# Kernel optimization log

Measured on AMD Instinct MI355X. Metric: run time of the kernel, lower is better.

Reference implementation:

```python
import jax, jax.numpy as jnp
import numpy as np

L, B, D = 4096, 4, 512  # seq_len, batch, embed_dim (nhead=1 so kdim=vdim=D)


def setup_inputs() -> dict:
    key = jax.random.key(0)
    ks = jax.random.split(key, 11)
    sc = 1.0 / np.sqrt(D)
    return {
        "x": jax.random.normal(ks[0], (L, B, D), jnp.float32),
        "e": jax.random.normal(ks[1], (L, B, D), jnp.float32),
        "relay": jax.random.normal(ks[2], (1, B, D), jnp.float32),
        "Wq": jax.random.normal(ks[3], (D, D), jnp.float32) * sc,
        "bq": jax.random.normal(ks[4], (D,), jnp.float32) * sc,
        "Wk": jax.random.normal(ks[5], (D, D), jnp.float32) * sc,
        "bk": jax.random.normal(ks[6], (D,), jnp.float32) * sc,
        "Wv": jax.random.normal(ks[7], (D, D), jnp.float32) * sc,
        "bv": jax.random.normal(ks[8], (D,), jnp.float32) * sc,
        "Wo": jax.random.normal(ks[9], (D, D), jnp.float32) * sc,
        "bo": jax.random.normal(ks[10], (D,), jnp.float32) * sc,
    }


def _window3(t):
    # t: [L,B,D] -> [L,B,3,D] with zero padding at the sequence boundaries
    # (matches nn.Unfold(kernel=[3,1], padding=[1,0]): positions l-1, l, l+1)
    n = t.shape[0]
    tp = jnp.pad(t, ((1, 1), (0, 0), (0, 0)))
    return jnp.stack([tp[:n], tp[1:n + 1], tp[2:n + 2]], axis=2)


def reference(x, e, relay, Wq, bq, Wk, bk, Wv, bv, Wo, bo):
    l, b, d = x.shape
    scale = 1.0 / jnp.sqrt(jnp.asarray(d, x.dtype))

    q = x @ Wq.T + bq          # [L,B,D]
    k = x @ Wk.T + bk
    v = x @ Wv.T + bv

    # cores = [embedding tokens e ; relay broadcast over L]  -> [2,L,B,D]
    s = jnp.broadcast_to(relay, (l, b, d))
    cores = jnp.stack([e, s], axis=0)
    k_c = cores @ Wk.T + bk    # [2,L,B,D]
    v_c = cores @ Wv.T + bv

    # ring (local windowed) attention: window = [k_{l-1},k_l,k_{l+1}, k(e_l), k(relay)]
    kw = jnp.concatenate([_window3(k), jnp.transpose(k_c, (1, 2, 0, 3))], axis=2)  # [L,B,5,D]
    vw = jnp.concatenate([_window3(v), jnp.transpose(v_c, (1, 2, 0, 3))], axis=2)  # [L,B,5,D]
    logits = jnp.einsum('lbd,lbwd->lbw', q, kw) * scale
    alphas = jax.nn.softmax(logits, axis=2)
    ring = jnp.einsum('lbw,lbwd->lbd', alphas, vw)  # [L,B,D]

    # star (relay) attention: query is the UNprojected relay token (as in source)
    k_r = relay @ Wk.T + bk    # [1,B,D]
    v_r = relay @ Wv.T + bv
    kk = jnp.concatenate([k, k_r], axis=0)  # [L+1,B,D]
    vv = jnp.concatenate([v, v_r], axis=0)
    s_logits = jnp.einsum('obd,nbd->bon', relay, kk) * scale  # [B,1,L+1]
    s_alphas = jax.nn.softmax(s_logits, axis=-1)
    star = jnp.einsum('bon,nbd->obd', s_alphas, vv)  # [1,B,D]

    return (ring @ Wo.T + bo, star @ Wo.T + bo)
```

## Files before the change

kernel.cpp:

```cpp
#include <hip/hip_runtime.h>
#include <hip/hip_fp16.h>

#define L_SEQ 4096
#define BATCH 4
#define DIM 512
#define M_ROWS (L_SEQ * BATCH)
#define SCALE 0.04419417382415922f
#define SLS 4097

typedef __attribute__((ext_vector_type(4))) float f32x4;
typedef __attribute__((ext_vector_type(8))) _Float16 f16x8;
typedef __attribute__((ext_vector_type(4))) _Float16 f16x4;

__device__ inline void gload16(const void* g, void* l) {
    __builtin_amdgcn_global_load_lds(
        (const __attribute__((address_space(1))) void*)g,
        (__attribute__((address_space(3))) void*)l, 16, 0, 0);
}

__device__ inline float wred_sum(float s) {
#pragma unroll
    for (int o = 32; o; o >>= 1) s += __shfl_xor(s, o);
    return s;
}
__device__ inline float wred_max(float s) {
#pragma unroll
    for (int o = 32; o; o >>= 1) s = fmaxf(s, __shfl_xor(s, o));
    return s;
}

#define PREP_NV   1048576
#define PREP_XE_B 8192
#define PREP_W_B  768
__global__ __launch_bounds__(256) void prep(
    const float* __restrict__ x, const float* __restrict__ e,
    const float* __restrict__ Wq, const float* __restrict__ Wk,
    const float* __restrict__ Wv, const float* __restrict__ Wo,
    const float* __restrict__ bq, const float* __restrict__ bk, const float* __restrict__ bv,
    const float* __restrict__ relay,
    _Float16* __restrict__ xh, _Float16* __restrict__ eh,
    _Float16* __restrict__ Wqkv, _Float16* __restrict__ Wof, float* __restrict__ bqkv,
    float* __restrict__ krvr, float* __restrict__ star)
{
    const int bid = blockIdx.x;
    if (bid < PREP_XE_B) {
        int j = bid * 256 + threadIdx.x;
        const float* src; _Float16* dst;
        if (j < PREP_NV) { src = x; dst = xh; } else { src = e; dst = eh; j -= PREP_NV; }
        const float* p = src + (size_t)j * 8;
        float4 a = *(const float4*)p, b = *(const float4*)(p + 4);
        f16x8 h = { (_Float16)a.x, (_Float16)a.y, (_Float16)a.z, (_Float16)a.w,
                    (_Float16)b.x, (_Float16)b.y, (_Float16)b.z, (_Float16)b.w };
        *(f16x8*)(dst + (size_t)j * 8) = h;
    } else if (bid < PREP_XE_B + PREP_W_B) {
        const int w = (bid - PREP_XE_B) * 256 + threadIdx.x;
        const int o = w * 4, r = o >> 9, c = o & 511;
        const float* W = (r < 512) ? Wq : (r < 1024 ? Wk : Wv);
        float4 v = *(const float4*)(W + (size_t)(r & 511) * 512 + c);
        *(f16x4*)(Wqkv + o) = f16x4{ (_Float16)v.x, (_Float16)v.y, (_Float16)v.z, (_Float16)v.w };
        if (o < 262144) {
            float4 u = *(const float4*)(Wo + o);
            *(f16x4*)(Wof + o) = f16x4{ (_Float16)u.x, (_Float16)u.y, (_Float16)u.z, (_Float16)u.w };
        }
        if (w < 1536) bqkv[w] = (w < 512) ? bq[w] : (w < 1024 ? bk[w - 512] : bv[w - 1024]);
    } else {
        const int o = ((bid - PREP_XE_B - PREP_W_B) << 2) + (threadIdx.x >> 6);
        const int lane = threadIdx.x & 63;
        const int sel = o >> 11, rem = o & 2047, b = rem >> 9, j = rem & 511;
        const float* W = sel ? Wv : Wk;
        const float* wr = W + (size_t)j * 512 + lane * 8;
        const float* rp = relay + (size_t)b * 512 + lane * 8;
        float4 w0 = *(const float4*)wr,  w1 = *(const float4*)(wr + 4);
        float4 r0 = *(const float4*)rp,  r1 = *(const float4*)(rp + 4);
        float s = w0.x * r0.x + w0.y * r0.y + w0.z * r0.z + w0.w * r0.w
                + w1.x * r1.x + w1.y * r1.y + w1.z * r1.z + w1.w * r1.w;
        s = wred_sum(s);
        if (lane == 0) {
            krvr[o] = s + (sel ? bv[j] : bk[j]);
            if (o < 2048) star[o] = 0.f;
        }
    }
}

struct GemmP {
    const _Float16* A;
    const _Float16* W;
    const float*    bias;
    void*           C;
    int             cstride;
    int             ncols;
};

template<int OUT16>
__global__ __launch_bounds__(256) void gemm2p(GemmP g0, GemmP g1, int n0, int cpx)
{
    __shared__ __align__(16) char smem[49152];
    _Float16* lAb = (_Float16*)smem;
    _Float16* lBb = (_Float16*)(smem + 24576);

    const int bid = blockIdx.x;
    const int swz = (bid & 7) * cpx + (bid >> 3);
    const GemmP g = (swz < n0) ? g0 : g1;
    const int l  = (swz < n0) ? swz : swz - n0;
    const int mt = l / g.ncols, nt = l % g.ncols;
    const int row0 = mt * 128, col0 = nt * 128;

    const int tid = threadIdx.x;
    const int wave = tid >> 6, lane = tid & 63;
    const int wm = (wave >> 1) * 64, wn = (wave & 1) * 64;

    f32x4 acc[4][4];
#pragma unroll
    for (int i = 0; i < 4; ++i)
#pragma unroll
        for (int j = 0; j < 4; ++j) acc[i][j] = (f32x4)0.f;

    const int idx0 = tid, idx1 = 256 + tid;
    const int r0_ = idx0 >> 2, c0_ = ((idx0 & 3) ^ ((idx0 >> 3) & 3)) * 8;
    const int r1_ = idx1 >> 2, c1_ = ((idx1 & 3) ^ ((idx1 >> 3) & 3)) * 8;
    const int ldsb0 = (wave * 64) * 8;
    const int ldsb1 = (256 + wave * 64) * 8;

    auto stage = [&](int buf, int t) {
        const int k0 = t << 5;
        gload16(g.A + (size_t)(row0 + r0_) * 512 + k0 + c0_, lAb + buf * 4096 + ldsb0);
        gload16(g.A + (size_t)(row0 + r1_) * 512 + k0 + c1_, lAb + buf * 4096 + ldsb1);
        gload16(g.W + (size_t)(col0 + r0_) * 512 + k0 + c0_, lBb + buf * 4096 + ldsb0);
        gload16(g.W + (size_t)(col0 + r1_) * 512 + k0 + c1_, lBb + buf * 4096 + ldsb1);
    };
    stage(0, 0);
    stage(1, 1);
    stage(2, 2);

    const int rslot = ((lane >> 4) ^ ((lane >> 1) & 3)) * 8;
    const int arb = (wm + (lane & 15)) * 32 + rslot;
    const int brb = (wn + (lane & 15)) * 32 + rslot;

    int rs = 0;
#pragma unroll 1
    for (int t = 0; t < 16; ++t) {
        if (t < 14)       asm volatile("s_waitcnt vmcnt(8)" ::: "memory");
        else if (t == 14) asm volatile("s_waitcnt vmcnt(4)" ::: "memory");
        else              asm volatile("s_waitcnt vmcnt(0)" ::: "memory");
        __builtin_amdgcn_s_barrier();
        f16x8 af[4], bfr[4];
#pragma unroll
        for (int i = 0; i < 4; ++i) af[i]  = *(const f16x8*)(lAb + rs * 4096 + arb + i * 512);
#pragma unroll
        for (int i = 0; i < 4; ++i) bfr[i] = *(const f16x8*)(lBb + rs * 4096 + brb + i * 512);
        __builtin_amdgcn_s_setprio(1);
#pragma unroll
        for (int mi = 0; mi < 4; ++mi)
#pragma unroll
            for (int ni = 0; ni < 4; ++ni)
                acc[mi][ni] = __builtin_amdgcn_mfma_f32_16x16x32_f16(
                    af[mi], bfr[ni], acc[mi][ni], 0, 0, 0);
        __builtin_amdgcn_s_setprio(0);
        asm volatile("s_waitcnt lgkmcnt(0)" ::: "memory");
        __builtin_amdgcn_s_barrier();
        if (t + 3 < 16) stage(rs, t + 3);
        rs = (rs == 2) ? 0 : rs + 1;
    }

    const int h = lane >> 4, c = lane & 15;
    if (OUT16) {
        _Float16* ep = (_Float16*)smem;
#pragma unroll
        for (int mi = 0; mi < 4; ++mi)
#pragma unroll
            for (int ni = 0; ni < 4; ++ni) {
                const float bb = g.bias[col0 + wn + ni * 16 + c];
#pragma unroll
                for (int r = 0; r < 4; ++r)
                    ep[(wm + mi * 16 + h * 4 + r) * 136 + wn + ni * 16 + c] =
                        (_Float16)(acc[mi][ni][r] + bb);
            }
        __syncthreads();
        const int rt = tid >> 4, ct = (tid & 15) * 8;
#pragma unroll
        for (int j = 0; j < 8; ++j) {
            const int row = j * 16 + rt;
            f16x8 v = *(const f16x8*)(ep + row * 136 + ct);
            *(f16x8*)((_Float16*)g.C + (size_t)(row0 + row) * g.cstride + col0 + ct) = v;
        }
    } else {
        float* ep = (float*)smem;
#pragma unroll
        for (int pass = 0; pass < 2; ++pass) {
            if ((wm == 0) == (pass == 0)) {
#pragma unroll
                for (int mi = 0; mi < 4; ++mi)
#pragma unroll
                    for (int ni = 0; ni < 4; ++ni) {
                        const float bb = g.bias[col0 + wn + ni * 16 + c];
#pragma unroll
                        for (int r = 0; r < 4; ++r)
                            ep[(mi * 16 + h * 4 + r) * 132 + wn + ni * 16 + c] =
                                acc[mi][ni][r] + bb;
                    }
            }
            __syncthreads();
            const int rt = tid >> 5, ct4 = (tid & 31) * 4;
#pragma unroll
            for (int j = 0; j < 8; ++j) {
                const int row = j * 8 + rt;
                f32x4 v = *(const f32x4*)(ep + row * 132 + ct4);
                *(f32x4*)((float*)g.C + (size_t)(row0 + pass * 64 + row) * g.cstride + col0 + ct4) = v;
            }
            if (pass == 0) __syncthreads();
        }
    }
}

__global__ __launch_bounds__(256) void tail_fused(GemmP g,
    const float* __restrict__ star, const float* __restrict__ Wo,
    const float* __restrict__ bo, float* __restrict__ out1)
{
    __shared__ __align__(16) char smem[49152];
    const int bid = blockIdx.x;
    const int tid = threadIdx.x;
    const int lane = tid & 63;

    if (bid >= 512) {
        const int o = ((bid - 512) << 2) + (tid >> 6);
        const int b = o >> 9, j = o & 511;
        const float* sp = star + (size_t)b * 512 + lane * 8;
        const float* wr = Wo + (size_t)j * 512 + lane * 8;
        float4 w0 = *(const float4*)wr,  w1 = *(const float4*)(wr + 4);
        float4 s0 = *(const float4*)sp,  s1 = *(const float4*)(sp + 4);
        float s = w0.x * s0.x + w0.y * s0.y + w0.z * s0.z + w0.w * s0.w
                + w1.x * s1.x + w1.y * s1.y + w1.z * s1.z + w1.w * s1.w;
        s = wred_sum(s);
        if (lane == 0) out1[o] = s + bo[j];
        return;
    }

    _Float16* lAb = (_Float16*)smem;
    _Float16* lBb = (_Float16*)(smem + 24576);

    const int swz = (bid & 7) * 64 + (bid >> 3);
    const int mt = swz / g.ncols, nt = swz % g.ncols;
    const int row0 = mt * 128, col0 = nt * 128;

    const int wave = tid >> 6;
    const int wm = (wave >> 1) * 64, wn = (wave & 1) * 64;

    f32x4 acc[4][4];
#pragma unroll
    for (int i = 0; i < 4; ++i)
#pragma unroll
        for (int j = 0; j < 4; ++j) acc[i][j] = (f32x4)0.f;

    const int idx0 = tid, idx1 = 256 + tid;
    const int r0_ = idx0 >> 2, c0_ = ((idx0 & 3) ^ ((idx0 >> 3) & 3)) * 8;
    const int r1_ = idx1 >> 2, c1_ = ((idx1 & 3) ^ ((idx1 >> 3) & 3)) * 8;
    const int ldsb0 = (wave * 64) * 8;
    const int ldsb1 = (256 + wave * 64) * 8;

    auto stage = [&](int buf, int t) {
        const int k0 = t << 5;
        gload16(g.A + (size_t)(row0 + r0_) * 512 + k0 + c0_, lAb + buf * 4096 + ldsb0);
        gload16(g.A + (size_t)(row0 + r1_) * 512 + k0 + c1_, lAb + buf * 4096 + ldsb1);
        gload16(g.W + (size_t)(col0 + r0_) * 512 + k0 + c0_, lBb + buf * 4096 + ldsb0);
        gload16(g.W + (size_t)(col0 + r1_) * 512 + k0 + c1_, lBb + buf * 4096 + ldsb1);
    };
    stage(0, 0);
    stage(1, 1);
    stage(2, 2);

    const int rslot = ((lane >> 4) ^ ((lane >> 1) & 3)) * 8;
    const int arb = (wm + (lane & 15)) * 32 + rslot;
    const int brb = (wn + (lane & 15)) * 32 + rslot;

    int rs = 0;
#pragma unroll 1
    for (int t = 0; t < 16; ++t) {
        if (t < 14)       asm volatile("s_waitcnt vmcnt(8)" ::: "memory");
        else if (t == 14) asm volatile("s_waitcnt vmcnt(4)" ::: "memory");
        else              asm volatile("s_waitcnt vmcnt(0)" ::: "memory");
        __builtin_amdgcn_s_barrier();
        f16x8 af[4], bfr[4];
#pragma unroll
        for (int i = 0; i < 4; ++i) af[i]  = *(const f16x8*)(lAb + rs * 4096 + arb + i * 512);
#pragma unroll
        for (int i = 0; i < 4; ++i) bfr[i] = *(const f16x8*)(lBb + rs * 4096 + brb + i * 512);
        __builtin_amdgcn_s_setprio(1);
#pragma unroll
        for (int mi = 0; mi < 4; ++mi)
#pragma unroll
            for (int ni = 0; ni < 4; ++ni)
                acc[mi][ni] = __builtin_amdgcn_mfma_f32_16x16x32_f16(
                    af[mi], bfr[ni], acc[mi][ni], 0, 0, 0);
        __builtin_amdgcn_s_setprio(0);
        asm volatile("s_waitcnt lgkmcnt(0)" ::: "memory");
        __builtin_amdgcn_s_barrier();
        if (t + 3 < 16) stage(rs, t + 3);
        rs = (rs == 2) ? 0 : rs + 1;
    }

    const int h = lane >> 4, c = lane & 15;
    float* ep = (float*)smem;
#pragma unroll
    for (int pass = 0; pass < 2; ++pass) {
        if ((wm == 0) == (pass == 0)) {
#pragma unroll
            for (int mi = 0; mi < 4; ++mi)
#pragma unroll
                for (int ni = 0; ni < 4; ++ni) {
                    const float bb = g.bias[col0 + wn + ni * 16 + c];
#pragma unroll
                    for (int r = 0; r < 4; ++r)
                        ep[(mi * 16 + h * 4 + r) * 132 + wn + ni * 16 + c] =
                            acc[mi][ni][r] + bb;
                }
        }
        __syncthreads();
        const int rt = tid >> 5, ct4 = (tid & 31) * 4;
#pragma unroll
        for (int j = 0; j < 8; ++j) {
            const int row = j * 8 + rt;
            f32x4 v = *(const f32x4*)(ep + row * 132 + ct4);
            *(f32x4*)((float*)g.C + (size_t)(row0 + pass * 64 + row) * g.cstride + col0 + ct4) = v;
        }
        if (pass == 0) __syncthreads();
    }
}

__global__ __launch_bounds__(256) void ring_attn(
    const _Float16* __restrict__ qkv,
    const _Float16* __restrict__ ekv,
    const float* __restrict__ krvr,
    const float* __restrict__ relay,
    _Float16* __restrict__ ring,
    float* __restrict__ slog)
{
    const int wid = (blockIdx.x << 2) + (threadIdx.x >> 6);
    const int lane = threadIdx.x & 63;
    const int r = wid, b = r & 3, l = r >> 2;
    const int d0 = lane << 3;

    float q[8], rl[8];
    {
        f16x8 t = *(const f16x8*)(qkv + (size_t)r * 1536 + d0);
#pragma unroll
        for (int i = 0; i < 8; ++i) q[i] = (float)t[i];
        const float* rp = relay + (size_t)b * 512 + d0;
        float4 a = *(const float4*)rp, c = *(const float4*)(rp + 4);
        rl[0] = a.x; rl[1] = a.y; rl[2] = a.z; rl[3] = a.w;
        rl[4] = c.x; rl[5] = c.y; rl[6] = c.z; rl[7] = c.w;
    }
    const bool has0 = (l > 0), has2 = (l < L_SEQ - 1);

    auto dotk = [&](const _Float16* kp) -> float {
        f16x8 t = *(const f16x8*)(kp + d0);
        float s = 0.f;
#pragma unroll
        for (int i = 0; i < 8; ++i) s += q[i] * (float)t[i];
        return wred_sum(s);
    };

    float lg[5];
    lg[0] = has0 ? dotk(qkv + (size_t)(r - 4) * 1536 + 512) : 0.f;
    lg[2] = has2 ? dotk(qkv + (size_t)(r + 4) * 1536 + 512) : 0.f;
    lg[3] = dotk(ekv + (size_t)r * 1024);
    {
        f16x8 t = *(const f16x8*)(qkv + (size_t)r * 1536 + 512 + d0);
        float s1 = 0.f, s2 = 0.f;
#pragma unroll
        for (int i = 0; i < 8; ++i) { float kf = (float)t[i]; s1 += q[i] * kf; s2 += rl[i] * kf; }
#pragma unroll
        for (int o = 32; o; o >>= 1) { s1 += __shfl_xor(s1, o); s2 += __shfl_xor(s2, o); }
        lg[1] = s1;
        if (lane == 0) slog[(size_t)b * SLS + l] = s2 * SCALE;
    }
    {
        const float* kp = krvr + (size_t)b * 512 + d0;
        float s = 0.f;
#pragma unroll
        for (int i = 0; i < 8; ++i) s += q[i] * kp[i];
        lg[4] = wred_sum(s);
    }

    float li[5], m = -1e30f;
#pragma unroll
    for (int w = 0; w < 5; ++w) { li[w] = lg[w] * SCALE; m = fmaxf(m, li[w]); }
    float ew[5], Z = 0.f;
#pragma unroll
    for (int w = 0; w < 5; ++w) { ew[w] = expf(li[w] - m); Z += ew[w]; }
    const float inv = 1.f / Z;

    float o8[8] = {0, 0, 0, 0, 0, 0, 0, 0};
    auto addv = [&](const _Float16* vp, float a) {
        f16x8 t = *(const f16x8*)(vp + d0);
#pragma unroll
        for (int i = 0; i < 8; ++i) o8[i] += a * (float)t[i];
    };
    if (has0) addv(qkv + (size_t)(r - 4) * 1536 + 1024, ew[0] * inv);
    addv(qkv + (size_t)r * 1536 + 1024, ew[1] * inv);
    if (has2) addv(qkv + (size_t)(r + 4) * 1536 + 1024, ew[2] * inv);
    addv(ekv + (size_t)r * 1024 + 512, ew[3] * inv);
    {
        const float* vp = krvr + 2048 + (size_t)b * 512 + d0;
        const float a = ew[4] * inv;
#pragma unroll
        for (int i = 0; i < 8; ++i) o8[i] += a * vp[i];
    }
    f16x8 res;
#pragma unroll
    for (int i = 0; i < 8; ++i) res[i] = (_Float16)o8[i];
    *(f16x8*)(ring + (size_t)r * 512 + d0) = res;
}

__global__ __launch_bounds__(1024) void star_softmax(
    const float* __restrict__ relay, const float* __restrict__ krvr,
    float* __restrict__ slog)
{
    const int b = blockIdx.x, t = threadIdx.x, lane = t & 63, w = t >> 6;
    __shared__ float red[16];
    __shared__ float bc[2];
    float* sl = slog + (size_t)b * SLS;

    float p = 0.f;
    if (t < 512) p = relay[(size_t)b * 512 + t] * krvr[(size_t)b * 512 + t];
    p = wred_sum(p);
    if (lane == 0) red[w] = p;
    __syncthreads();
    if (t == 0) { float s = 0.f; for (int i = 0; i < 16; ++i) s += red[i]; bc[0] = s * SCALE; }
    __syncthreads();
    const float selfl = bc[0];
    __syncthreads();

    float v[4];
#pragma unroll
    for (int i = 0; i < 4; ++i) v[i] = sl[t + i * 1024];

    float m = selfl;
#pragma unroll
    for (int i = 0; i < 4; ++i) m = fmaxf(m, v[i]);
    m = wred_max(m);
    if (lane == 0) red[w] = m;
    __syncthreads();
    if (t == 0) { float mm = red[0]; for (int i = 1; i < 16; ++i) mm = fmaxf(mm, red[i]); bc[1] = mm; }
    __syncthreads();
    m = bc[1];

    float ev[4], z = (t == 0) ? expf(selfl - m) : 0.f;
#pragma unroll
    for (int i = 0; i < 4; ++i) { ev[i] = expf(v[i] - m); z += ev[i]; }
    z = wred_sum(z);
    if (lane == 0) red[w] = z;
    __syncthreads();
    if (t == 0) { float s = 0.f; for (int i = 0; i < 16; ++i) s += red[i]; bc[0] = 1.f / s; }
    __syncthreads();
    const float inv = bc[0];

#pragma unroll
    for (int i = 0; i < 4; ++i) sl[t + i * 1024] = ev[i] * inv;
    if (t == 0) sl[SLS - 1] = expf(selfl - m) * inv;
}

__global__ __launch_bounds__(256) void star_out(
    const float* __restrict__ slog, const _Float16* __restrict__ qkv,
    const float* __restrict__ krvr, float* __restrict__ star)
{
    const int b = threadIdx.x >> 6, lane = threadIdx.x & 63;
    const int chunk = blockIdx.x;
    const int d0 = lane << 3;
    const float* al = slog + (size_t)b * SLS;
    float acc[8] = {0, 0, 0, 0, 0, 0, 0, 0};
#pragma unroll 4
    for (int i = 0; i < 64; ++i) {
        const int n = chunk * 64 + i;
        const float a = al[n];
        f16x8 v = *(const f16x8*)(qkv + (size_t)(n * 4 + b) * 1536 + 1024 + d0);
#pragma unroll
        for (int j = 0; j < 8; ++j) acc[j] += a * (float)v[j];
    }
    if (chunk == 63) {
        const float a = al[SLS - 1];
        const float* vr = krvr + 2048 + (size_t)b * 512 + d0;
#pragma unroll
        for (int j = 0; j < 8; ++j) acc[j] += a * vr[j];
    }
#pragma unroll
    for (int j = 0; j < 8; ++j) atomicAdd(&star[(size_t)b * 512 + d0 + j], acc[j]);
}

extern "C" void kernel_launch(void* const* d_in, const int* in_sizes, int n_in,
                              void* d_out, int out_size, void* d_ws, size_t ws_size,
                              hipStream_t stream) {
    const float* x     = (const float*)d_in[0];
    const float* e     = (const float*)d_in[1];
    const float* relay = (const float*)d_in[2];
    const float* Wq    = (const float*)d_in[3];
    const float* bq    = (const float*)d_in[4];
    const float* Wk    = (const float*)d_in[5];
    const float* bk    = (const float*)d_in[6];
    const float* Wv    = (const float*)d_in[7];
    const float* bv    = (const float*)d_in[8];
    const float* Wo    = (const float*)d_in[9];
    const float* bo    = (const float*)d_in[10];
    float* out = (float*)d_out;

    size_t off = 0;
    auto alloc = [&](size_t bytes) {
        void* p = (char*)d_ws + off;
        off += (bytes + 255) & ~(size_t)255;
        return p;
    };
    _Float16* Wqkv = (_Float16*)alloc((size_t)1536 * 512 * 2);
    _Float16* Wof  = (_Float16*)alloc((size_t)512 * 512 * 2);
    float*    bqkv = (float*)   alloc(1536 * 4);
    _Float16* xh   = (_Float16*)alloc((size_t)M_ROWS * 512 * 2);
    _Float16* eh   = (_Float16*)alloc((size_t)M_ROWS * 512 * 2);
    _Float16* qkv  = (_Float16*)alloc((size_t)M_ROWS * 1536 * 2);
    _Float16* ekv  = (_Float16*)alloc((size_t)M_ROWS * 1024 * 2);
    float*    krvr = (float*)   alloc(2 * 4 * 512 * 4);
    float*    slog = (float*)   alloc((size_t)4 * SLS * 4);
    float*    star = (float*)   alloc(4 * 512 * 4);
    _Float16* ringb = xh;

    prep<<<PREP_XE_B + PREP_W_B + 1024, 256, 0, stream>>>(
        x, e, Wq, Wk, Wv, Wo, bq, bk, bv, relay,
        xh, eh, Wqkv, Wof, bqkv, krvr, star);

    GemmP gq { xh, Wqkv,                     bqkv,       qkv, 1536, 12 };
    GemmP ge { eh, Wqkv + (size_t)512 * 512, bqkv + 512, ekv, 1024,  8 };
    gemm2p<1><<<2560, 256, 0, stream>>>(gq, ge, 1536, 320);

    ring_attn<<<M_ROWS / 4, 256, 0, stream>>>(qkv, ekv, krvr, relay, ringb, slog);

    star_softmax<<<4, 1024, 0, stream>>>(relay, krvr, slog);
    star_out<<<64, 256, 0, stream>>>(slog, qkv, krvr, star);

    GemmP go { ringb, Wof, bo, out, 512, 4 };
    tail_fused<<<1024, 256, 0, stream>>>(go, star, Wo, bo, out + (size_t)M_ROWS * 512);
}
```

Measured before the change: 151.1 us.

## Fuse fp32-to-fp16 activation conversion into QKV GEMM A-tile loading

Removes the separate prep pass that converted x and e to fp16. The QKV GEMM now loads fp32 A tiles into registers, converts them, and writes them to LDS inside a restructured three-slot software pipeline, while B tiles still use direct global-to-LDS loads. This avoids a full write and re-read of the fp16 activations. The cost is twice the global bytes for A in every GEMM tile, since each A row is re-read once per column tile, plus extra register pressure from the staged A buffers.

```diff
diff --git a/kernel.cpp b/kernel.cpp
--- a/kernel.cpp
+++ b/kernel.cpp
@@ -29,31 +29,17 @@
     return s;
 }
 
-#define PREP_NV   1048576
-#define PREP_XE_B 8192
-#define PREP_W_B  768
 __global__ __launch_bounds__(256) void prep(
-    const float* __restrict__ x, const float* __restrict__ e,
     const float* __restrict__ Wq, const float* __restrict__ Wk,
     const float* __restrict__ Wv, const float* __restrict__ Wo,
     const float* __restrict__ bq, const float* __restrict__ bk, const float* __restrict__ bv,
     const float* __restrict__ relay,
-    _Float16* __restrict__ xh, _Float16* __restrict__ eh,
     _Float16* __restrict__ Wqkv, _Float16* __restrict__ Wof, float* __restrict__ bqkv,
     float* __restrict__ krvr, float* __restrict__ star)
 {
     const int bid = blockIdx.x;
-    if (bid < PREP_XE_B) {
-        int j = bid * 256 + threadIdx.x;
-        const float* src; _Float16* dst;
-        if (j < PREP_NV) { src = x; dst = xh; } else { src = e; dst = eh; j -= PREP_NV; }
-        const float* p = src + (size_t)j * 8;
-        float4 a = *(const float4*)p, b = *(const float4*)(p + 4);
-        f16x8 h = { (_Float16)a.x, (_Float16)a.y, (_Float16)a.z, (_Float16)a.w,
-                    (_Float16)b.x, (_Float16)b.y, (_Float16)b.z, (_Float16)b.w };
-        *(f16x8*)(dst + (size_t)j * 8) = h;
-    } else if (bid < PREP_XE_B + PREP_W_B) {
-        const int w = (bid - PREP_XE_B) * 256 + threadIdx.x;
+    if (bid < 768) {
+        const int w = bid * 256 + threadIdx.x;
         const int o = w * 4, r = o >> 9, c = o & 511;
         const float* W = (r < 512) ? Wq : (r < 1024 ? Wk : Wv);
         float4 v = *(const float4*)(W + (size_t)(r & 511) * 512 + c);
@@ -64,7 +50,7 @@
         }
         if (w < 1536) bqkv[w] = (w < 512) ? bq[w] : (w < 1024 ? bk[w - 512] : bv[w - 1024]);
     } else {
-        const int o = ((bid - PREP_XE_B - PREP_W_B) << 2) + (threadIdx.x >> 6);
+        const int o = ((bid - 768) << 2) + (threadIdx.x >> 6);
         const int lane = threadIdx.x & 63;
         const int sel = o >> 11, rem = o & 2047, b = rem >> 9, j = rem & 511;
         const float* W = sel ? Wv : Wk;
@@ -83,7 +69,7 @@
 }
 
 struct GemmP {
-    const _Float16* A;
+    const void*     A;
     const _Float16* W;
     const float*    bias;
     void*           C;
@@ -108,6 +94,7 @@
     const int tid = threadIdx.x;
     const int wave = tid >> 6, lane = tid & 63;
     const int wm = (wave >> 1) * 64, wn = (wave & 1) * 64;
+    const float* Af = (const float*)g.A;
 
     f32x4 acc[4][4];
 #pragma unroll
@@ -115,39 +102,57 @@
 #pragma unroll
         for (int j = 0; j < 4; ++j) acc[i][j] = (f32x4)0.f;
 
-    const int idx0 = tid, idx1 = 256 + tid;
-    const int r0_ = idx0 >> 2, c0_ = ((idx0 & 3) ^ ((idx0 >> 3) & 3)) * 8;
+    const int idx1 = 256 + tid;
+    const int r0_ = tid >> 2,  c0_ = ((tid & 3) ^ ((tid >> 3) & 3)) * 8;
     const int r1_ = idx1 >> 2, c1_ = ((idx1 & 3) ^ ((idx1 >> 3) & 3)) * 8;
     const int ldsb0 = (wave * 64) * 8;
     const int ldsb1 = (256 + wave * 64) * 8;
 
-    auto stage = [&](int buf, int t) {
+    auto stageB = [&](int slot, int t) {
         const int k0 = t << 5;
-        gload16(g.A + (size_t)(row0 + r0_) * 512 + k0 + c0_, lAb + buf * 4096 + ldsb0);
-        gload16(g.A + (size_t)(row0 + r1_) * 512 + k0 + c1_, lAb + buf * 4096 + ldsb1);
-        gload16(g.W + (size_t)(col0 + r0_) * 512 + k0 + c0_, lBb + buf * 4096 + ldsb0);
-        gload16(g.W + (size_t)(col0 + r1_) * 512 + k0 + c1_, lBb + buf * 4096 + ldsb1);
-    };
-    stage(0, 0);
-    stage(1, 1);
-    stage(2, 2);
+        gload16(g.W + (size_t)(col0 + r0_) * 512 + k0 + c0_, lBb + slot * 4096 + ldsb0);
+        gload16(g.W + (size_t)(col0 + r1_) * 512 + k0 + c1_, lBb + slot * 4096 + ldsb1);
+    };
+    f32x4 a0[4], a1[4], a2[4];
+    auto loadA = [&](f32x4* d, int t) {
+        const int k0 = t << 5;
+        const float* p0 = Af + (size_t)(row0 + r0_) * 512 + k0 + c0_;
+        const float* p1 = Af + (size_t)(row0 + r1_) * 512 + k0 + c1_;
+        d[0] = *(const f32x4*)p0; d[1] = *(const f32x4*)(p0 + 4);
+        d[2] = *(const f32x4*)p1; d[3] = *(const f32x4*)(p1 + 4);
+    };
+    auto writeA = [&](const f32x4* s, int slot) {
+        f16x8 h0 = { (_Float16)s[0][0], (_Float16)s[0][1], (_Float16)s[0][2], (_Float16)s[0][3],
+                     (_Float16)s[1][0], (_Float16)s[1][1], (_Float16)s[1][2], (_Float16)s[1][3] };
+        f16x8 h1 = { (_Float16)s[2][0], (_Float16)s[2][1], (_Float16)s[2][2], (_Float16)s[2][3],
+                     (_Float16)s[3][0], (_Float16)s[3][1], (_Float16)s[3][2], (_Float16)s[3][3] };
+        *(f16x8*)(lAb + slot * 4096 + tid * 8) = h0;
+        *(f16x8*)(lAb + slot * 4096 + (256 + tid) * 8) = h1;
+    };
+
+    stageB(0, 0); stageB(1, 1); stageB(2, 2);
+    asm volatile("" ::: "memory");
+    loadA(a0, 0); asm volatile("" ::: "memory");
+    loadA(a1, 1); asm volatile("" ::: "memory");
+    loadA(a2, 2);
+    asm volatile("s_waitcnt vmcnt(8)" ::: "memory");
+    writeA(a0, 0);
+    asm volatile("s_waitcnt lgkmcnt(0)" ::: "memory");
 
     const int rslot = ((lane >> 4) ^ ((lane >> 1) & 3)) * 8;
     const int arb = (wm + (lane & 15)) * 32 + rslot;
     const int brb = (wn + (lane & 15)) * 32 + rslot;
 
-    int rs = 0;
-#pragma unroll 1
-    for (int t = 0; t < 16; ++t) {
-        if (t < 14)       asm volatile("s_waitcnt vmcnt(8)" ::: "memory");
-        else if (t == 14) asm volatile("s_waitcnt vmcnt(4)" ::: "memory");
-        else              asm volatile("s_waitcnt vmcnt(0)" ::: "memory");
+    auto step = [&](int t, int slot, int swrt, f32x4* aW, f32x4* aL) {
+        if (t == 0)      asm volatile("s_waitcnt vmcnt(4)" ::: "memory");
+        else if (t < 14) asm volatile("s_waitcnt vmcnt(6)" ::: "memory");
+        else             asm volatile("s_waitcnt vmcnt(0)" ::: "memory");
         __builtin_amdgcn_s_barrier();
         f16x8 af[4], bfr[4];
 #pragma unroll
-        for (int i = 0; i < 4; ++i) af[i]  = *(const f16x8*)(lAb + rs * 4096 + arb + i * 512);
-#pragma unroll
-        for (int i = 0; i < 4; ++i) bfr[i] = *(const f16x8*)(lBb + rs * 4096 + brb + i * 512);
+        for (int i = 0; i < 4; ++i) af[i]  = *(const f16x8*)(lAb + slot * 4096 + arb + i * 512);
+#pragma unroll
+        for (int i = 0; i < 4; ++i) bfr[i] = *(const f16x8*)(lBb + slot * 4096 + brb + i * 512);
         __builtin_amdgcn_s_setprio(1);
 #pragma unroll
         for (int mi = 0; mi < 4; ++mi)
@@ -156,11 +161,22 @@
                 acc[mi][ni] = __builtin_amdgcn_mfma_f32_16x16x32_f16(
                     af[mi], bfr[ni], acc[mi][ni], 0, 0, 0);
         __builtin_amdgcn_s_setprio(0);
+        if (t < 15) writeA(aW, swrt);
         asm volatile("s_waitcnt lgkmcnt(0)" ::: "memory");
         __builtin_amdgcn_s_barrier();
-        if (t + 3 < 16) stage(rs, t + 3);
-        rs = (rs == 2) ? 0 : rs + 1;
-    }
+        if (t <= 12) {
+            stageB(slot, t + 3);
+            asm volatile("" ::: "memory");
+            loadA(aL, t + 3);
+        }
+    };
+#pragma unroll 1
+    for (int tb = 0; tb < 15; tb += 3) {
+        step(tb,     0, 1, a1, a0);
+        step(tb + 1, 1, 2, a2, a1);
+        step(tb + 2, 2, 0, a0, a2);
+    }
+    step(15, 0, 1, a1, a0);
 
     const int h = lane >> 4, c = lane & 15;
     if (OUT16) {
@@ -237,6 +253,7 @@
 
     _Float16* lAb = (_Float16*)smem;
     _Float16* lBb = (_Float16*)(smem + 24576);
+    const _Float16* Ah = (const _Float16*)g.A;
 
     const int swz = (bid & 7) * 64 + (bid >> 3);
     const int mt = swz / g.ncols, nt = swz % g.ncols;
@@ -259,8 +276,8 @@
 
     auto stage = [&](int buf, int t) {
         const int k0 = t << 5;
-        gload16(g.A + (size_t)(row0 + r0_) * 512 + k0 + c0_, lAb + buf * 4096 + ldsb0);
-        gload16(g.A + (size_t)(row0 + r1_) * 512 + k0 + c1_, lAb + buf * 4096 + ldsb1);
+        gload16(Ah + (size_t)(row0 + r0_) * 512 + k0 + c0_, lAb + buf * 4096 + ldsb0);
+        gload16(Ah + (size_t)(row0 + r1_) * 512 + k0 + c1_, lAb + buf * 4096 + ldsb1);
         gload16(g.W + (size_t)(col0 + r0_) * 512 + k0 + c0_, lBb + buf * 4096 + ldsb0);
         gload16(g.W + (size_t)(col0 + r1_) * 512 + k0 + c1_, lBb + buf * 4096 + ldsb1);
     };
@@ -511,21 +528,19 @@
     _Float16* Wqkv = (_Float16*)alloc((size_t)1536 * 512 * 2);
     _Float16* Wof  = (_Float16*)alloc((size_t)512 * 512 * 2);
     float*    bqkv = (float*)   alloc(1536 * 4);
-    _Float16* xh   = (_Float16*)alloc((size_t)M_ROWS * 512 * 2);
-    _Float16* eh   = (_Float16*)alloc((size_t)M_ROWS * 512 * 2);
     _Float16* qkv  = (_Float16*)alloc((size_t)M_ROWS * 1536 * 2);
     _Float16* ekv  = (_Float16*)alloc((size_t)M_ROWS * 1024 * 2);
+    _Float16* ringb= (_Float16*)alloc((size_t)M_ROWS * 512 * 2);
     float*    krvr = (float*)   alloc(2 * 4 * 512 * 4);
     float*    slog = (float*)   alloc((size_t)4 * SLS * 4);
     float*    star = (float*)   alloc(4 * 512 * 4);
-    _Float16* ringb = xh;
-
-    prep<<<PREP_XE_B + PREP_W_B + 1024, 256, 0, stream>>>(
-        x, e, Wq, Wk, Wv, Wo, bq, bk, bv, relay,
-        xh, eh, Wqkv, Wof, bqkv, krvr, star);
-
-    GemmP gq { xh, Wqkv,                     bqkv,       qkv, 1536, 12 };
-    GemmP ge { eh, Wqkv + (size_t)512 * 512, bqkv + 512, ekv, 1024,  8 };
+
+    prep<<<768 + 1024, 256, 0, stream>>>(
+        Wq, Wk, Wv, Wo, bq, bk, bv, relay,
+        Wqkv, Wof, bqkv, krvr, star);
+
+    GemmP gq { x, Wqkv,                     bqkv,       qkv, 1536, 12 };
+    GemmP ge { e, Wqkv + (size_t)512 * 512, bqkv + 512, ekv, 1024,  8 };
     gemm2p<1><<<2560, 256, 0, stream>>>(gq, ge, 1536, 320);
 
     ring_attn<<<M_ROWS / 4, 256, 0, stream>>>(qkv, ekv, krvr, relay, ringb, slog);
```

Result: no change. 149.4 us (-1.1%).
